# Kernel optimization log

Hardware: AMD Instinct MI355X
Metric: run time of the kernel (lower is better)

The kernel has to match this reference:

```python
import jax, jax.numpy as jnp
import numpy as np

D_MODEL = 2048
N_HEADS = 16
HEAD_DIM = D_MODEL // N_HEADS
B, T = 2, 2048


def setup_inputs() -> dict:
    key = jax.random.key(0)
    ks = jax.random.split(key, 7)
    s = 0.02
    return {
        "x": jax.random.normal(ks[0], (B, T, D_MODEL), dtype=jnp.float32),
        "w_qkv": jax.random.normal(ks[1], (D_MODEL, 3 * D_MODEL), dtype=jnp.float32) * s,
        "w_proj": jax.random.normal(ks[2], (D_MODEL, D_MODEL), dtype=jnp.float32) * s,
        "w_ff1": jax.random.normal(ks[3], (D_MODEL, 4 * D_MODEL), dtype=jnp.float32) * s,
        "b_ff1": jnp.zeros((4 * D_MODEL,), dtype=jnp.float32),
        "w_ff2": jax.random.normal(ks[4], (4 * D_MODEL, D_MODEL), dtype=jnp.float32) * s,
        "b_ff2": jnp.zeros((D_MODEL,), dtype=jnp.float32),
    }


def reference(x, w_qkv, w_proj, w_ff1, b_ff1, w_ff2, b_ff2):
    Bs, Ts, C = x.shape
    H, hd = N_HEADS, HEAD_DIM
    # fused qkv projection
    qkv = jnp.einsum("btc,cd->btd", x, w_qkv)
    q, k, v = jnp.split(qkv, 3, axis=-1)
    # (B, T, C) -> (B, H, T, hd)
    q = q.reshape(Bs, Ts, H, hd).transpose(0, 2, 1, 3)
    k = k.reshape(Bs, Ts, H, hd).transpose(0, 2, 1, 3)
    v = v.reshape(Bs, Ts, H, hd).transpose(0, 2, 1, 3)
    # paged KV write + gather round-trip (empty cache, n_kv_head == n_heads)
    # is the identity on k, v; attention is causal SDPA over the full cache.
    scale = 1.0 / jnp.sqrt(jnp.asarray(hd, dtype=x.dtype))
    scores = jnp.einsum("bhqd,bhkd->bhqk", q, k) * scale
    causal = jnp.tril(jnp.ones((Ts, Ts), dtype=bool))
    scores = jnp.where(causal, scores, jnp.finfo(scores.dtype).min)
    attn = jax.nn.softmax(scores, axis=-1)
    out = jnp.einsum("bhqk,bhkd->bhqd", attn, v)  # (B, H, T, hd)
    out = out.transpose(0, 2, 1, 3).reshape(Bs, Ts, C)
    attn_out = jnp.einsum("btc,cd->btd", out, w_proj)
    # feed-forward with exact GELU (torch nn.GELU default)
    h = jax.nn.gelu(jnp.einsum("btc,cf->btf", x, w_ff1) + b_ff1, approximate=False)
    ff_out = jnp.einsum("btf,fc->btc", h, w_ff2) + b_ff2
    return x + attn_out + ff_out
```

## Files before the change

### kernel.cpp

```cpp
#include <hip/hip_runtime.h>
#include <hip/hip_bf16.h>
#include <cmath>

typedef __bf16 bf16x8 __attribute__((ext_vector_type(8)));
typedef float f32x4 __attribute__((ext_vector_type(4)));
typedef unsigned short u16;
typedef unsigned int u32;

#define DEV __device__ __forceinline__

static constexpr int BB = 2;
static constexpr int T = 2048;
static constexpr int DM = 2048;
static constexpr int NH = 16;
static constexpr int HD = 128;
static constexpr int FF = 8192;
static constexpr int M = BB * T;
static constexpr int NQKV = 3 * DM;

DEV u16 f2b(float f) {
  u32 u = __builtin_bit_cast(u32, f);
  u = (u + 0x7FFFu + ((u >> 16) & 1u)) >> 16;
  return (u16)u;
}
DEV float b2f(u16 h) {
  u32 u = ((u32)h) << 16;
  return __builtin_bit_cast(float, u);
}

DEV void gload16(const u16* g, const u16* l) {
  __builtin_amdgcn_global_load_lds(
      (const __attribute__((address_space(1))) void*)(uintptr_t)g,
      (__attribute__((address_space(3))) void*)(unsigned)(uintptr_t)l,
      16, 0, 0);
}


__global__ void cvt_f32_to_bf16(const float* __restrict__ in, u16* __restrict__ out, int n4) {
  int i = blockIdx.x * blockDim.x + threadIdx.x;
  if (i >= n4) return;
  float4 v = reinterpret_cast<const float4*>(in)[i];
  ushort4 o;
  o.x = f2b(v.x); o.y = f2b(v.y); o.z = f2b(v.z); o.w = f2b(v.w);
  reinterpret_cast<ushort4*>(out)[i] = o;
}

__global__ void transpose_cvt(const float* __restrict__ W, u16* __restrict__ Wt, int K, int N) {
  __shared__ float tile[32][33];
  int nb = blockIdx.x * 32, kb = blockIdx.y * 32;
  int r = threadIdx.x >> 3;
  int c4 = (threadIdx.x & 7) * 4;
  float4 v = *reinterpret_cast<const float4*>(&W[(size_t)(kb + r) * N + nb + c4]);
  tile[r][c4] = v.x; tile[r][c4 + 1] = v.y; tile[r][c4 + 2] = v.z; tile[r][c4 + 3] = v.w;
  __syncthreads();
  ushort4 o;
  o.x = f2b(tile[c4][r]);     o.y = f2b(tile[c4 + 1][r]);
  o.z = f2b(tile[c4 + 2][r]); o.w = f2b(tile[c4 + 3][r]);
  *reinterpret_cast<ushort4*>(&Wt[(size_t)(nb + r) * K + kb + c4]) = o;
}

__global__ void ff2_reduce(const float* __restrict__ p0, const float* __restrict__ p1,
                           const float* __restrict__ bias, const float* __restrict__ x,
                           const u16* __restrict__ ap, float* __restrict__ out) {
  int i = blockIdx.x * blockDim.x + threadIdx.x;
  float4 a = reinterpret_cast<const float4*>(p0)[i];
  float4 b = reinterpret_cast<const float4*>(p1)[i];
  float4 xx = reinterpret_cast<const float4*>(x)[i];
  float4 bi = reinterpret_cast<const float4*>(bias)[i & (DM / 4 - 1)];
  ushort4 a4 = reinterpret_cast<const ushort4*>(ap)[i];
  float4 o;
  o.x = a.x + b.x + bi.x + xx.x + b2f(a4.x);
  o.y = a.y + b.y + bi.y + xx.y + b2f(a4.y);
  o.z = a.z + b.z + bi.z + xx.z + b2f(a4.z);
  o.w = a.w + b.w + bi.w + xx.w + b2f(a4.w);
  reinterpret_cast<float4*>(out)[i] = o;
}

template <int EPI>
__global__ __launch_bounds__(512, 2) void gemm8(
    const u16* __restrict__ A, const u16* __restrict__ Bt, int Ndim,
    int Kstride, int Klen, int gx, int tpp,
    u16* __restrict__ out_bf, float* __restrict__ p0, float* __restrict__ p1,
    const float* __restrict__ bias) {
  __shared__ __align__(16) u16 lds[2 * 32768];
  const int t = threadIdx.x;
  const int nwg = gridDim.x, cpx = nwg >> 3;
  const int wg = (blockIdx.x & 7) * cpx + (blockIdx.x >> 3);
  const int part = wg / tpp, tid = wg % tpp;
  const int m0 = (tid / gx) * 256, n0 = (tid % gx) * 256;
  const int wave = t >> 6, lane = t & 63;
  const int wm = wave >> 2, wn = wave & 3;
  const int lr = lane & 15, lk = lane >> 4;

  const int srow = t >> 3;
  const int sc8 = ((t & 7) ^ (srow & 7)) * 8;
  const u16* gA = &A[(size_t)(m0 + srow) * Kstride + (size_t)part * Klen + sc8];
  const u16* gB = &Bt[(size_t)(n0 + srow) * Kstride + (size_t)part * Klen + sc8];
  const int wls = wave * 512;

  u16* buf0 = lds;
  u16* buf1 = lds + 32768;

#define STAGE_A(buf, h, kt)                                                      \
  {                                                                              \
    gload16(gA + (size_t)((h) * 128) * Kstride + (kt) * 64,                      \
            (buf) + (h) * 8192 + wls);                                           \
    gload16(gA + (size_t)((h) * 128 + 64) * Kstride + (kt) * 64,                 \
            (buf) + (h) * 8192 + 4096 + wls);                                    \
  }
#define STAGE_B(buf, h, kt)                                                      \
  {                                                                              \
    gload16(gB + (size_t)((h) * 128) * Kstride + (kt) * 64,                      \
            (buf) + 16384 + (h) * 8192 + wls);                                   \
    gload16(gB + (size_t)((h) * 128 + 64) * Kstride + (kt) * 64,                 \
            (buf) + 16384 + (h) * 8192 + 4096 + wls);                            \
  }
#define PH_PRE                          \
  __builtin_amdgcn_sched_barrier(0);    \
  __builtin_amdgcn_s_barrier();         \
  __builtin_amdgcn_sched_barrier(0);    \
  __builtin_amdgcn_s_setprio(1);
#define PH_POST                         \
  __builtin_amdgcn_s_setprio(0);        \
  __builtin_amdgcn_sched_barrier(0);    \
  __builtin_amdgcn_s_barrier();         \
  __builtin_amdgcn_sched_barrier(0);

  const int NT = Klen >> 6;

  STAGE_A(buf0, 0, 0); STAGE_A(buf0, 1, 0);
  STAGE_B(buf0, 0, 0); STAGE_B(buf0, 1, 0);
  STAGE_A(buf1, 0, 1); STAGE_B(buf1, 0, 1);
  __builtin_amdgcn_sched_barrier(0);
  asm volatile("s_waitcnt vmcnt(4)" ::: "memory");
  __builtin_amdgcn_s_barrier();
  __builtin_amdgcn_sched_barrier(0);

  f32x4 acc[8][4] = {};
  const int aBase = (wm * 128 + lr) * 64;
  const int bBase = 16384 + (wn * 64 + lr) * 64;
  const int c0 = (lk ^ (lr & 7)) * 8;
  const int c1 = ((4 + lk) ^ (lr & 7)) * 8;

  u16* cur = buf0;
  u16* alt = buf1;
  bf16x8 af[4][2], bq0[2][2], bq1[2][2];

  for (int kt = 0; kt < NT; ++kt) {
#pragma unroll
    for (int i = 0; i < 4; ++i) {
      af[i][0] = *(const bf16x8*)&cur[aBase + i * 1024 + c0];
      af[i][1] = *(const bf16x8*)&cur[aBase + i * 1024 + c1];
    }
#pragma unroll
    for (int j = 0; j < 2; ++j) {
      bq0[j][0] = *(const bf16x8*)&cur[bBase + j * 1024 + c0];
      bq0[j][1] = *(const bf16x8*)&cur[bBase + j * 1024 + c1];
    }
    if (kt + 1 < NT) STAGE_A(alt, 1, kt + 1);
    PH_PRE;
#pragma unroll
    for (int i = 0; i < 4; ++i)
#pragma unroll
      for (int j = 0; j < 2; ++j)
#pragma unroll
        for (int kk = 0; kk < 2; ++kk)
          acc[i][j] = __builtin_amdgcn_mfma_f32_16x16x32_bf16(af[i][kk], bq0[j][kk], acc[i][j], 0, 0, 0);
    PH_POST;
#pragma unroll
    for (int j = 0; j < 2; ++j) {
      bq1[j][0] = *(const bf16x8*)&cur[bBase + (2 + j) * 1024 + c0];
      bq1[j][1] = *(const bf16x8*)&cur[bBase + (2 + j) * 1024 + c1];
    }
    if (kt + 1 < NT) STAGE_B(alt, 1, kt + 1);
    PH_PRE;
#pragma unroll
    for (int i = 0; i < 4; ++i)
#pragma unroll
      for (int j = 0; j < 2; ++j)
#pragma unroll
        for (int kk = 0; kk < 2; ++kk)
          acc[i][2 + j] = __builtin_amdgcn_mfma_f32_16x16x32_bf16(af[i][kk], bq1[j][kk], acc[i][2 + j], 0, 0, 0);
    PH_POST;
#pragma unroll
    for (int i = 0; i < 4; ++i) {
      af[i][0] = *(const bf16x8*)&cur[aBase + (4 + i) * 1024 + c0];
      af[i][1] = *(const bf16x8*)&cur[aBase + (4 + i) * 1024 + c1];
    }
    if (kt + 2 < NT) STAGE_A(cur, 0, kt + 2);
    PH_PRE;
#pragma unroll
    for (int i = 0; i < 4; ++i)
#pragma unroll
      for (int j = 0; j < 2; ++j)
#pragma unroll
        for (int kk = 0; kk < 2; ++kk)
          acc[4 + i][2 + j] = __builtin_amdgcn_mfma_f32_16x16x32_bf16(af[i][kk], bq1[j][kk], acc[4 + i][2 + j], 0, 0, 0);
    PH_POST;
    if (kt + 2 < NT) STAGE_B(cur, 0, kt + 2);
    PH_PRE;
#pragma unroll
    for (int i = 0; i < 4; ++i)
#pragma unroll
      for (int j = 0; j < 2; ++j)
#pragma unroll
        for (int kk = 0; kk < 2; ++kk)
          acc[4 + i][j] = __builtin_amdgcn_mfma_f32_16x16x32_bf16(af[i][kk], bq0[j][kk], acc[4 + i][j], 0, 0, 0);
    __builtin_amdgcn_s_setprio(0);
    __builtin_amdgcn_sched_barrier(0);
    if (kt + 2 < NT)      asm volatile("s_waitcnt vmcnt(4)" ::: "memory");
    else if (kt + 1 < NT) asm volatile("s_waitcnt vmcnt(0)" ::: "memory");
    __builtin_amdgcn_s_barrier();
    __builtin_amdgcn_sched_barrier(0);
    u16* tmp = cur; cur = alt; alt = tmp;
  }
#undef STAGE_A
#undef STAGE_B
#undef PH_PRE
#undef PH_POST

  float* pout = (part == 0) ? p0 : p1;
#pragma unroll
  for (int i = 0; i < 8; ++i) {
#pragma unroll
    for (int j = 0; j < 4; ++j) {
#pragma unroll
      for (int r = 0; r < 4; ++r) {
        int gr = m0 + wm * 128 + i * 16 + (lane >> 4) * 4 + r;
        int gc = n0 + wn * 64 + j * 16 + (lane & 15);
        float v = acc[i][j][r];
        if constexpr (EPI == 0) {
          int part_ = gc >> 11, cc = gc & 2047;
          int head = cc >> 7, d = cc & 127;
          int b = gr >> 11, tt = gr & 2047;
          out_bf[(size_t)part_ * M * DM + (((size_t)(b * NH + head) * T + tt) * HD + d)] = f2b(v);
        } else if constexpr (EPI == 2) {
          v += bias[gc];
          float u = v * (v * v * 0.044715f + 1.0f) * 0.7978845608028654f;
          float e = exp2f(u * 2.885390081777927f);
          float th = 1.0f - 2.0f / (e + 1.0f);
          v = 0.5f * v * (1.0f + th);
          out_bf[(size_t)gr * Ndim + gc] = f2b(v);
        } else {
          pout[(size_t)gr * Ndim + gc] = v;
        }
      }
    }
  }
}

template <int EPI>
__global__ __launch_bounds__(512, 4) void gemm_bf16(
    const u16* __restrict__ A, const u16* __restrict__ Bt, int Ndim, int K, int gx,
    u16* __restrict__ out_bf, float* __restrict__ out_f32,
    const float* __restrict__ bias,
    const float* __restrict__ resid_f32, const u16* __restrict__ resid_bf) {
  __shared__ __align__(16) u16 lds[3 * (256 + 128) * 32];
  const int t = threadIdx.x;
  const int nwg = gridDim.x, cpx = nwg >> 3;
  const int wg = (blockIdx.x & 7) * cpx + (blockIdx.x >> 3);
  const int m0 = (wg / gx) * 256, n0 = (wg % gx) * 128;
  const int wave = t >> 6, lane = t & 63;
  const int wm = wave >> 1, wn = wave & 1;
  const int lr = lane & 15, lk = lane >> 4;

  u16* cA = lds;                   u16* cB = lds + 8192;
  u16* nA = lds + 12288;           u16* nB = lds + 12288 + 8192;
  u16* sA = lds + 2 * 12288;       u16* sB = lds + 2 * 12288 + 8192;

  const int sk = ((lane & 3) ^ ((lane >> 3) & 3)) * 8;
  const u16* gA0 = &A[(size_t)(m0 + wave * 16 + (lane >> 2)) * K + sk];
  const u16* gA1 = gA0 + (size_t)128 * K;
  const u16* gB0 = &Bt[(size_t)(n0 + wave * 16 + (lane >> 2)) * K + sk];

  const int wbase = wave * 512;

  auto stage = [&](u16* dA, u16* dB) {
    gload16(gA0, dA + wbase);
    gload16(gA1, dA + 4096 + wbase);
    gload16(gB0, dB + wbase);
    gA0 += 32; gA1 += 32; gB0 += 32;
  };

  const int NT = K >> 5;

  stage(cA, cB);
  stage(nA, nB);
  __builtin_amdgcn_sched_barrier(0);
  asm volatile("s_waitcnt vmcnt(3)" ::: "memory");
  __builtin_amdgcn_s_barrier();
  __builtin_amdgcn_sched_barrier(0);

  f32x4 acc[4][4] = {};
  const int rcol = (lk ^ ((lr >> 1) & 3)) * 8;

  for (int kt = 0; kt < NT; ++kt) {
    if (kt + 2 < NT) stage(sA, sB);
    bf16x8 af[4], bfr[4];
#pragma unroll
    for (int i = 0; i < 4; ++i) {
      af[i]  = *reinterpret_cast<const bf16x8*>(&cA[(wm * 64 + i * 16 + lr) * 32 + rcol]);
      bfr[i] = *reinterpret_cast<const bf16x8*>(&cB[(wn * 64 + i * 16 + lr) * 32 + rcol]);
    }
#pragma unroll
    for (int i = 0; i < 4; ++i)
#pragma unroll
      for (int j = 0; j < 4; ++j)
        acc[i][j] = __builtin_amdgcn_mfma_f32_16x16x32_bf16(af[i], bfr[j], acc[i][j], 0, 0, 0);
    if (kt + 1 < NT) {
      __builtin_amdgcn_sched_barrier(0);
      if (kt + 2 < NT) asm volatile("s_waitcnt vmcnt(3)" ::: "memory");
      else             asm volatile("s_waitcnt vmcnt(0)" ::: "memory");
      __builtin_amdgcn_s_barrier();
      __builtin_amdgcn_sched_barrier(0);
      u16* tA = cA; u16* tB = cB;
      cA = nA; cB = nB; nA = sA; nB = sB; sA = tA; sB = tB;
    }
  }

#pragma unroll
  for (int i = 0; i < 4; ++i) {
#pragma unroll
    for (int j = 0; j < 4; ++j) {
#pragma unroll
      for (int r = 0; r < 4; ++r) {
        int gr = m0 + wm * 64 + i * 16 + (lane >> 4) * 4 + r;
        int gc = n0 + wn * 64 + j * 16 + (lane & 15);
        float v = acc[i][j][r];
        if constexpr (EPI == 1) {
          out_bf[(size_t)gr * Ndim + gc] = f2b(v);
        } else if constexpr (EPI == 3) {
          v += bias[gc] + resid_f32[(size_t)gr * Ndim + gc] + b2f(resid_bf[(size_t)gr * Ndim + gc]);
          out_f32[(size_t)gr * Ndim + gc] = v;
        } else {
          int hh = gr >> 7, d = gr & 127;
          int b = gc >> 11, tt = gc & 2047;
          out_bf[((size_t)(b * NH + hh) * HD + d) * T + tt] = f2b(v);
        }
      }
    }
  }
}

__global__ __launch_bounds__(256) void attn_fwd(
    const u16* __restrict__ qg, const u16* __restrict__ kg,
    const u16* __restrict__ vt, u16* __restrict__ outg) {
  __shared__ __align__(16) u16 lK[2][64 * 128];
  __shared__ __align__(16) u16 lVt[2][128 * 64];
  __shared__ __align__(16) u16 lP[4][16 * 72];
  const int t = threadIdx.x;
  const int qi = gridDim.x - 1 - blockIdx.x;
  const int bh = blockIdx.y;
  const int wv = t >> 6, lane = t & 63;
  const int lc = lane & 15, lg = lane >> 4;
  const size_t base = (size_t)bh * T * HD;
  const size_t vbase = (size_t)bh * HD * T;
  const int q0 = qi * 64;

  bf16x8 qf[4];
#pragma unroll
  for (int kk = 0; kk < 4; ++kk)
    qf[kk] = *reinterpret_cast<const bf16x8*>(
        &qg[base + (size_t)(q0 + wv * 16 + lc) * HD + kk * 32 + lg * 8]);

  f32x4 oacc[8] = {};
  float mrow[4], lrow[4];
#pragma unroll
  for (int r = 0; r < 4; ++r) { mrow[r] = -INFINITY; lrow[r] = 0.f; }

  auto stageKV = [&](int kt, int b) {
#pragma unroll
    for (int h = 0; h < 4; ++h) {
      int c = t + h * 256;
      int row = c >> 4;
      int sb = ((c & 15) * 16) ^ ((row & 7) << 4);
      gload16(&kg[base + (size_t)(kt * 64 + row) * HD + (sb >> 1)],
              (const u16*)((const char*)lK[b] + (h * 256 + wv * 64) * 16));
    }
#pragma unroll
    for (int h = 0; h < 4; ++h) {
      int c = t + h * 256;
      int row = c >> 3;
      int sb = ((c & 7) * 16) ^ ((row & 7) << 4);
      gload16(&vt[vbase + (size_t)row * T + kt * 64 + (sb >> 1)],
              (const u16*)((const char*)lVt[b] + (h * 256 + wv * 64) * 16));
    }
  };

  const float scaleL = 0.08838834764831845f * 1.4426950408889634f;
  const int ntiles = qi + 1;

  stageKV(0, 0);
  __builtin_amdgcn_sched_barrier(0);
  asm volatile("s_waitcnt vmcnt(0)" ::: "memory");
  __builtin_amdgcn_s_barrier();
  __builtin_amdgcn_sched_barrier(0);

  for (int kt = 0; kt < ntiles; ++kt) {
    const int cb = kt & 1;
    if (kt + 1 < ntiles) stageKV(kt + 1, cb ^ 1);
    const u16* lKc = lK[cb];
    const u16* lVc = lVt[cb];

    f32x4 s[4] = {};
    __builtin_amdgcn_s_setprio(1);
#pragma unroll
    for (int nf = 0; nf < 4; ++nf) {
      int krow = nf * 16 + lc;
#pragma unroll
      for (int kk = 0; kk < 4; ++kk) {
        int dbyte = kk * 64 + lg * 16;
        bf16x8 kf = *reinterpret_cast<const bf16x8*>(
            reinterpret_cast<const char*>(lKc) + krow * 256 + (dbyte ^ ((krow & 7) << 4)));
        s[nf] = __builtin_amdgcn_mfma_f32_16x16x32_bf16(qf[kk], kf, s[nf], 0, 0, 0);
      }
    }
    __builtin_amdgcn_s_setprio(0);

    float rmax[4];
#pragma unroll
    for (int r = 0; r < 4; ++r) rmax[r] = -INFINITY;
#pragma unroll
    for (int nf = 0; nf < 4; ++nf) {
      int col = kt * 64 + nf * 16 + lc;
#pragma unroll
      for (int r = 0; r < 4; ++r) {
        int row = q0 + wv * 16 + lg * 4 + r;
        float sv = s[nf][r] * scaleL;
        if (col > row) sv = -INFINITY;
        s[nf][r] = sv;
        rmax[r] = fmaxf(rmax[r], sv);
      }
    }
#pragma unroll
    for (int mk = 1; mk < 16; mk <<= 1)
#pragma unroll
      for (int r = 0; r < 4; ++r)
        rmax[r] = fmaxf(rmax[r], __shfl_xor(rmax[r], mk));

    int need = 0;
#pragma unroll
    for (int r = 0; r < 4; ++r) need |= (rmax[r] > mrow[r] + 11.5f) ? 1 : 0;
    if (__any(need)) {
      float corr[4];
#pragma unroll
      for (int r = 0; r < 4; ++r) {
        float mnew = fmaxf(mrow[r], rmax[r]);
        corr[r] = exp2f(mrow[r] - mnew);
        mrow[r] = mnew;
        lrow[r] *= corr[r];
      }
#pragma unroll
      for (int dc = 0; dc < 8; ++dc)
#pragma unroll
        for (int r = 0; r < 4; ++r) oacc[dc][r] *= corr[r];
    }

#pragma unroll
    for (int nf = 0; nf < 4; ++nf) {
#pragma unroll
      for (int r = 0; r < 4; ++r) {
        float p = exp2f(s[nf][r] - mrow[r]);
        lrow[r] += p;
        lP[wv][(lg * 4 + r) * 72 + nf * 16 + lc] = f2b(p);
      }
    }
    bf16x8 pa[2];
#pragma unroll
    for (int kk = 0; kk < 2; ++kk)
      pa[kk] = *reinterpret_cast<const bf16x8*>(&lP[wv][lc * 72 + kk * 32 + lg * 8]);
    __builtin_amdgcn_s_setprio(1);
#pragma unroll
    for (int dc = 0; dc < 8; ++dc) {
#pragma unroll
      for (int kk = 0; kk < 2; ++kk) {
        int vrow = dc * 16 + lc;
        int off = (kk * 64 + lg * 16) ^ ((vrow & 7) << 4);
        bf16x8 vf = *reinterpret_cast<const bf16x8*>(
            reinterpret_cast<const char*>(lVc) + vrow * 128 + off);
        oacc[dc] = __builtin_amdgcn_mfma_f32_16x16x32_bf16(pa[kk], vf, oacc[dc], 0, 0, 0);
      }
    }
    __builtin_amdgcn_s_setprio(0);

    __builtin_amdgcn_sched_barrier(0);
    if (kt + 1 < ntiles) asm volatile("s_waitcnt vmcnt(0)" ::: "memory");
    __builtin_amdgcn_s_barrier();
    __builtin_amdgcn_sched_barrier(0);
  }

#pragma unroll
  for (int mk = 1; mk < 16; mk <<= 1)
#pragma unroll
    for (int r = 0; r < 4; ++r) lrow[r] += __shfl_xor(lrow[r], mk);

  const int b = bh >> 4, hh = bh & 15;
#pragma unroll
  for (int dc = 0; dc < 8; ++dc)
#pragma unroll
    for (int r = 0; r < 4; ++r) {
      int tt = q0 + wv * 16 + lg * 4 + r;
      int d = dc * 16 + lc;
      float o = oacc[dc][r] / lrow[r];
      outg[(size_t)(b * T + tt) * DM + hh * HD + d] = f2b(o);
    }
}


extern "C" void kernel_launch(void* const* d_in, const int* in_sizes, int n_in,
                              void* d_out, int out_size, void* d_ws, size_t ws_size,
                              hipStream_t stream) {
  const float* x      = (const float*)d_in[0];
  const float* w_qkv  = (const float*)d_in[1];
  const float* w_proj = (const float*)d_in[2];
  const float* w_ff1  = (const float*)d_in[3];
  const float* b_ff1  = (const float*)d_in[4];
  const float* w_ff2  = (const float*)d_in[5];
  const float* b_ff2  = (const float*)d_in[6];
  float* out = (float*)d_out;

  u16* ws = (u16*)d_ws;
  size_t o = 0;
  u16* x_bf      = ws + o; o += (size_t)M * DM;
  u16* wqkv_t    = ws + o; o += (size_t)NQKV * DM;
  u16* wproj_t   = ws + o; o += (size_t)DM * DM;
  u16* wff1_t    = ws + o; o += (size_t)FF * DM;
  u16* wff2_t    = ws + o; o += (size_t)DM * FF;
  u16* attn_proj = ws + o; o += (size_t)M * DM;
  u16* qbuf      = ws + o;
  u16* kbuf      = qbuf + (size_t)M * DM;
  u16* vtbuf     = kbuf + (size_t)M * DM;
  u16* attn_out  = vtbuf + (size_t)M * DM;
  u16* hbuf      = qbuf;

  float* p0 = (float*)ws;
  float* p1 = (float*)wff1_t;

  cvt_f32_to_bf16<<<(M * DM / 4 + 255) / 256, 256, 0, stream>>>(x, x_bf, M * DM / 4);
  transpose_cvt<<<dim3(NQKV / 32, DM / 32), 256, 0, stream>>>(w_qkv, wqkv_t, DM, NQKV);
  transpose_cvt<<<dim3(DM / 32, DM / 32), 256, 0, stream>>>(w_proj, wproj_t, DM, DM);
  transpose_cvt<<<dim3(FF / 32, DM / 32), 256, 0, stream>>>(w_ff1, wff1_t, DM, FF);
  transpose_cvt<<<dim3(DM / 32, FF / 32), 256, 0, stream>>>(w_ff2, wff2_t, FF, DM);

  gemm8<0><<<256, 512, 0, stream>>>(x_bf, wqkv_t, 4096, DM, DM, 16, 256,
                                    qbuf, nullptr, nullptr, nullptr);

  gemm_bf16<4><<<256, 512, 0, stream>>>(
      wqkv_t + (size_t)4096 * DM, x_bf, M, DM, 32, vtbuf, nullptr, nullptr, nullptr, nullptr);

  attn_fwd<<<dim3(T / 64, BB * NH), 256, 0, stream>>>(qbuf, kbuf, vtbuf, attn_out);

  gemm_bf16<1><<<256, 512, 0, stream>>>(
      attn_out, wproj_t, DM, DM, 16, attn_proj, nullptr, nullptr, nullptr, nullptr);

  gemm8<2><<<512, 512, 0, stream>>>(x_bf, wff1_t, FF, DM, DM, 32, 512,
                                    hbuf, nullptr, nullptr, b_ff1);

  gemm8<5><<<256, 512, 0, stream>>>(hbuf, wff2_t, DM, FF, 4096, 8, 128,
                                    nullptr, p0, p1, nullptr);

  ff2_reduce<<<M * DM / 4 / 256, 256, 0, stream>>>(p0, p1, b_ff2, x, attn_proj, out);
}
```

Before: 646.4 us.

## Store Q/K/V in MFMA fragment layout and run LDS-free attention

The QKV and V-transpose GEMM epilogues now write Q, K and V directly in a pre-tiled 32x32 MFMA fragment order. This lets a new attention kernel load operands straight from global memory into registers with no LDS staging or barriers. Each wave works independently on 32 query rows, using 32x32x16 MFMAs and register shuffles to rebuild the P operand. The cost is that K/V tiles are no longer shared across waves through LDS, so global and L2 traffic goes up. The causal work split also changes to 32-row blocks per wave, with the grid launched as T/128 blocks.

```diff
diff --git a/kernel.cpp b/kernel.cpp
--- a/kernel.cpp
+++ b/kernel.cpp
@@ -4,6 +4,7 @@
 
 typedef __bf16 bf16x8 __attribute__((ext_vector_type(8)));
 typedef float f32x4 __attribute__((ext_vector_type(4)));
+typedef float f32x16 __attribute__((ext_vector_type(16)));
 typedef unsigned short u16;
 typedef unsigned int u32;
 
@@ -233,7 +234,10 @@
           int part_ = gc >> 11, cc = gc & 2047;
           int head = cc >> 7, d = cc & 127;
           int b = gr >> 11, tt = gr & 2047;
-          out_bf[(size_t)part_ * M * DM + (((size_t)(b * NH + head) * T + tt) * HD + d)] = f2b(v);
+          int bh = b * NH + head;
+          size_t addr = (((size_t)(bh * 64 + (tt >> 5)) * 8 + (d >> 4)) * 512)
+                        + ((tt & 31) + ((d >> 3) & 1) * 32) * 8 + (d & 7);
+          out_bf[(size_t)part_ * M * DM + addr] = f2b(v);
         } else if constexpr (EPI == 2) {
           v += bias[gc];
           float u = v * (v * v * 0.044715f + 1.0f) * 0.7978845608028654f;
@@ -335,175 +339,130 @@
         } else {
           int hh = gr >> 7, d = gr & 127;
           int b = gc >> 11, tt = gc & 2047;
-          out_bf[((size_t)(b * NH + hh) * HD + d) * T + tt] = f2b(v);
+          int bh = b * NH + hh;
+          size_t addr = (((size_t)(bh * 128 + (tt >> 4)) * 4 + (d >> 5)) * 512)
+                        + ((d & 31) + ((tt >> 3) & 1) * 32) * 8 + (tt & 7);
+          out_bf[addr] = f2b(v);
         }
       }
     }
   }
 }
 
-__global__ __launch_bounds__(256) void attn_fwd(
-    const u16* __restrict__ qg, const u16* __restrict__ kg,
-    const u16* __restrict__ vt, u16* __restrict__ outg) {
-  __shared__ __align__(16) u16 lK[2][64 * 128];
-  __shared__ __align__(16) u16 lVt[2][128 * 64];
-  __shared__ __align__(16) u16 lP[4][16 * 72];
-  const int t = threadIdx.x;
+__global__ __launch_bounds__(256) void attn_frag(
+    const u16* __restrict__ qf_, const u16* __restrict__ kf_,
+    const u16* __restrict__ vf_, u16* __restrict__ outg) {
+  const int l = threadIdx.x & 63;
+  const int wq = threadIdx.x >> 6;
+  const int bh = blockIdx.y;
   const int qi = gridDim.x - 1 - blockIdx.x;
-  const int bh = blockIdx.y;
-  const int wv = t >> 6, lane = t & 63;
-  const int lc = lane & 15, lg = lane >> 4;
-  const size_t base = (size_t)bh * T * HD;
-  const size_t vbase = (size_t)bh * HD * T;
-  const int q0 = qi * 64;
-
-  bf16x8 qf[4];
-#pragma unroll
-  for (int kk = 0; kk < 4; ++kk)
-    qf[kk] = *reinterpret_cast<const bf16x8*>(
-        &qg[base + (size_t)(q0 + wv * 16 + lc) * HD + kk * 32 + lg * 8]);
-
-  f32x4 oacc[8] = {};
-  float mrow[4], lrow[4];
-#pragma unroll
-  for (int r = 0; r < 4; ++r) { mrow[r] = -INFINITY; lrow[r] = 0.f; }
-
-  auto stageKV = [&](int kt, int b) {
-#pragma unroll
-    for (int h = 0; h < 4; ++h) {
-      int c = t + h * 256;
-      int row = c >> 4;
-      int sb = ((c & 15) * 16) ^ ((row & 7) << 4);
-      gload16(&kg[base + (size_t)(kt * 64 + row) * HD + (sb >> 1)],
-              (const u16*)((const char*)lK[b] + (h * 256 + wv * 64) * 16));
-    }
-#pragma unroll
-    for (int h = 0; h < 4; ++h) {
-      int c = t + h * 256;
-      int row = c >> 3;
-      int sb = ((c & 7) * 16) ^ ((row & 7) << 4);
-      gload16(&vt[vbase + (size_t)row * T + kt * 64 + (sb >> 1)],
-              (const u16*)((const char*)lVt[b] + (h * 256 + wv * 64) * 16));
-    }
-  };
-
+  const int qb = qi * 4 + wq;
+  const int h = l >> 5, ln = l & 31;
+  const int qrow = qb * 32 + ln;
+
+  const u16* qbase = qf_ + ((size_t)(bh * 64 + qb) * 8) * 512 + l * 8;
+  bf16x8 qf[8];
+#pragma unroll
+  for (int s = 0; s < 8; ++s)
+    qf[s] = *reinterpret_cast<const bf16x8*>(qbase + s * 512);
+
+  f32x16 acc0 = {}, acc1 = {}, acc2 = {}, acc3 = {};
+  float mrow = -INFINITY, lrow = 0.f;
   const float scaleL = 0.08838834764831845f * 1.4426950408889634f;
-  const int ntiles = qi + 1;
-
-  stageKV(0, 0);
-  __builtin_amdgcn_sched_barrier(0);
-  asm volatile("s_waitcnt vmcnt(0)" ::: "memory");
-  __builtin_amdgcn_s_barrier();
-  __builtin_amdgcn_sched_barrier(0);
+  const int ntiles = qb + 1;
 
   for (int kt = 0; kt < ntiles; ++kt) {
-    const int cb = kt & 1;
-    if (kt + 1 < ntiles) stageKV(kt + 1, cb ^ 1);
-    const u16* lKc = lK[cb];
-    const u16* lVc = lVt[cb];
-
-    f32x4 s[4] = {};
-    __builtin_amdgcn_s_setprio(1);
-#pragma unroll
-    for (int nf = 0; nf < 4; ++nf) {
-      int krow = nf * 16 + lc;
-#pragma unroll
-      for (int kk = 0; kk < 4; ++kk) {
-        int dbyte = kk * 64 + lg * 16;
-        bf16x8 kf = *reinterpret_cast<const bf16x8*>(
-            reinterpret_cast<const char*>(lKc) + krow * 256 + (dbyte ^ ((krow & 7) << 4)));
-        s[nf] = __builtin_amdgcn_mfma_f32_16x16x32_bf16(qf[kk], kf, s[nf], 0, 0, 0);
+    const u16* kbase = kf_ + ((size_t)(bh * 64 + kt) * 8) * 512 + l * 8;
+    f32x16 sa = {};
+#pragma unroll
+    for (int s = 0; s < 8; ++s) {
+      bf16x8 kf = *reinterpret_cast<const bf16x8*>(kbase + s * 512);
+      sa = __builtin_amdgcn_mfma_f32_32x32x16_bf16(kf, qf[s], sa, 0, 0, 0);
+    }
+
+    float p[16];
+    float lmax = -INFINITY;
+    const bool diag = (kt == qb);
+#pragma unroll
+    for (int r = 0; r < 16; ++r) {
+      float sv = sa[r] * scaleL;
+      if (diag) {
+        int kv = kt * 32 + (r & 3) + 8 * (r >> 2) + 4 * h;
+        if (kv > qrow) sv = -INFINITY;
       }
-    }
-    __builtin_amdgcn_s_setprio(0);
-
-    float rmax[4];
-#pragma unroll
-    for (int r = 0; r < 4; ++r) rmax[r] = -INFINITY;
-#pragma unroll
-    for (int nf = 0; nf < 4; ++nf) {
-      int col = kt * 64 + nf * 16 + lc;
-#pragma unroll
-      for (int r = 0; r < 4; ++r) {
-        int row = q0 + wv * 16 + lg * 4 + r;
-        float sv = s[nf][r] * scaleL;
-        if (col > row) sv = -INFINITY;
-        s[nf][r] = sv;
-        rmax[r] = fmaxf(rmax[r], sv);
+      p[r] = sv;
+      lmax = fmaxf(lmax, sv);
+    }
+    float rmax = fmaxf(lmax, __shfl_xor(lmax, 32));
+
+    if (__any(rmax > mrow + 11.5f)) {
+      float mnew = fmaxf(mrow, rmax);
+      float corr = exp2f(mrow - mnew);
+      mrow = mnew;
+      lrow *= corr;
+#pragma unroll
+      for (int r = 0; r < 16; ++r) {
+        float cr = __shfl(corr, (r & 3) + 8 * (r >> 2) + 4 * h);
+        acc0[r] *= cr; acc1[r] *= cr; acc2[r] *= cr; acc3[r] *= cr;
       }
     }
-#pragma unroll
-    for (int mk = 1; mk < 16; mk <<= 1)
-#pragma unroll
-      for (int r = 0; r < 4; ++r)
-        rmax[r] = fmaxf(rmax[r], __shfl_xor(rmax[r], mk));
-
-    int need = 0;
-#pragma unroll
-    for (int r = 0; r < 4; ++r) need |= (rmax[r] > mrow[r] + 11.5f) ? 1 : 0;
-    if (__any(need)) {
-      float corr[4];
-#pragma unroll
-      for (int r = 0; r < 4; ++r) {
-        float mnew = fmaxf(mrow[r], rmax[r]);
-        corr[r] = exp2f(mrow[r] - mnew);
-        mrow[r] = mnew;
-        lrow[r] *= corr[r];
-      }
-#pragma unroll
-      for (int dc = 0; dc < 8; ++dc)
-#pragma unroll
-        for (int r = 0; r < 4; ++r) oacc[dc][r] *= corr[r];
-    }
-
-#pragma unroll
-    for (int nf = 0; nf < 4; ++nf) {
-#pragma unroll
-      for (int r = 0; r < 4; ++r) {
-        float p = exp2f(s[nf][r] - mrow[r]);
-        lrow[r] += p;
-        lP[wv][(lg * 4 + r) * 72 + nf * 16 + lc] = f2b(p);
-      }
-    }
-    bf16x8 pa[2];
-#pragma unroll
-    for (int kk = 0; kk < 2; ++kk)
-      pa[kk] = *reinterpret_cast<const bf16x8*>(&lP[wv][lc * 72 + kk * 32 + lg * 8]);
-    __builtin_amdgcn_s_setprio(1);
-#pragma unroll
-    for (int dc = 0; dc < 8; ++dc) {
-#pragma unroll
-      for (int kk = 0; kk < 2; ++kk) {
-        int vrow = dc * 16 + lc;
-        int off = (kk * 64 + lg * 16) ^ ((vrow & 7) << 4);
-        bf16x8 vf = *reinterpret_cast<const bf16x8*>(
-            reinterpret_cast<const char*>(lVc) + vrow * 128 + off);
-        oacc[dc] = __builtin_amdgcn_mfma_f32_16x16x32_bf16(pa[kk], vf, oacc[dc], 0, 0, 0);
-      }
-    }
-    __builtin_amdgcn_s_setprio(0);
-
-    __builtin_amdgcn_sched_barrier(0);
-    if (kt + 1 < ntiles) asm volatile("s_waitcnt vmcnt(0)" ::: "memory");
-    __builtin_amdgcn_s_barrier();
-    __builtin_amdgcn_sched_barrier(0);
-  }
-
-#pragma unroll
-  for (int mk = 1; mk < 16; mk <<= 1)
-#pragma unroll
-    for (int r = 0; r < 4; ++r) lrow[r] += __shfl_xor(lrow[r], mk);
+
+    float ls = 0.f;
+#pragma unroll
+    for (int r = 0; r < 16; ++r) {
+      p[r] = exp2f(p[r] - mrow);
+      ls += p[r];
+    }
+    lrow += ls + __shfl_xor(ls, 32);
+
+    u32 w[8];
+#pragma unroll
+    for (int c = 0; c < 8; ++c)
+      asm("v_cvt_pk_bf16_f32 %0, %1, %2" : "=v"(w[c]) : "v"(p[2 * c]), "v"(p[2 * c + 1]));
+    u32 x[8];
+#pragma unroll
+    for (int c = 0; c < 8; ++c) x[c] = (u32)__shfl_xor((int)w[c], 32);
+    uint4 A0, A1;
+    A0.x = h ? x[2] : w[0]; A0.y = h ? x[3] : w[1];
+    A0.z = h ? w[2] : x[0]; A0.w = h ? w[3] : x[1];
+    A1.x = h ? x[6] : w[4]; A1.y = h ? x[7] : w[5];
+    A1.z = h ? w[6] : x[4]; A1.w = h ? w[7] : x[5];
+    bf16x8 pa0 = __builtin_bit_cast(bf16x8, A0);
+    bf16x8 pa1 = __builtin_bit_cast(bf16x8, A1);
+
+    const u16* vbase = vf_ + ((size_t)(bh * 128 + kt * 2) * 4) * 512 + l * 8;
+    bf16x8 v0, v1;
+    v0 = *reinterpret_cast<const bf16x8*>(vbase + 0 * 512);
+    v1 = *reinterpret_cast<const bf16x8*>(vbase + 4 * 512);
+    acc0 = __builtin_amdgcn_mfma_f32_32x32x16_bf16(pa0, v0, acc0, 0, 0, 0);
+    acc0 = __builtin_amdgcn_mfma_f32_32x32x16_bf16(pa1, v1, acc0, 0, 0, 0);
+    v0 = *reinterpret_cast<const bf16x8*>(vbase + 1 * 512);
+    v1 = *reinterpret_cast<const bf16x8*>(vbase + 5 * 512);
+    acc1 = __builtin_amdgcn_mfma_f32_32x32x16_bf16(pa0, v0, acc1, 0, 0, 0);
+    acc1 = __builtin_amdgcn_mfma_f32_32x32x16_bf16(pa1, v1, acc1, 0, 0, 0);
+    v0 = *reinterpret_cast<const bf16x8*>(vbase + 2 * 512);
+    v1 = *reinterpret_cast<const bf16x8*>(vbase + 6 * 512);
+    acc2 = __builtin_amdgcn_mfma_f32_32x32x16_bf16(pa0, v0, acc2, 0, 0, 0);
+    acc2 = __builtin_amdgcn_mfma_f32_32x32x16_bf16(pa1, v1, acc2, 0, 0, 0);
+    v0 = *reinterpret_cast<const bf16x8*>(vbase + 3 * 512);
+    v1 = *reinterpret_cast<const bf16x8*>(vbase + 7 * 512);
+    acc3 = __builtin_amdgcn_mfma_f32_32x32x16_bf16(pa0, v0, acc3, 0, 0, 0);
+    acc3 = __builtin_amdgcn_mfma_f32_32x32x16_bf16(pa1, v1, acc3, 0, 0, 0);
+  }
 
   const int b = bh >> 4, hh = bh & 15;
 #pragma unroll
-  for (int dc = 0; dc < 8; ++dc)
-#pragma unroll
-    for (int r = 0; r < 4; ++r) {
-      int tt = q0 + wv * 16 + lg * 4 + r;
-      int d = dc * 16 + lc;
-      float o = oacc[dc][r] / lrow[r];
-      outg[(size_t)(b * T + tt) * DM + hh * HD + d] = f2b(o);
-    }
+  for (int r = 0; r < 16; ++r) {
+    int qr = (r & 3) + 8 * (r >> 2) + 4 * h;
+    float lr = __shfl(lrow, qr);
+    float rl = 1.0f / lr;
+    int tt = qb * 32 + qr;
+    size_t rowoff = ((size_t)(b * T + tt)) * DM + hh * HD + ln;
+    outg[rowoff + 0]  = f2b(acc0[r] * rl);
+    outg[rowoff + 32] = f2b(acc1[r] * rl);
+    outg[rowoff + 64] = f2b(acc2[r] * rl);
+    outg[rowoff + 96] = f2b(acc3[r] * rl);
+  }
 }
 
 
@@ -548,7 +507,7 @@
   gemm_bf16<4><<<256, 512, 0, stream>>>(
       wqkv_t + (size_t)4096 * DM, x_bf, M, DM, 32, vtbuf, nullptr, nullptr, nullptr, nullptr);
 
-  attn_fwd<<<dim3(T / 64, BB * NH), 256, 0, stream>>>(qbuf, kbuf, vtbuf, attn_out);
+  attn_frag<<<dim3(T / 128, BB * NH), 256, 0, stream>>>(qbuf, kbuf, vtbuf, attn_out);
 
   gemm_bf16<1><<<256, 512, 0, stream>>>(
       attn_out, wproj_t, DM, DM, 16, attn_proj, nullptr, nullptr, nullptr, nullptr);
```

New measurement: 636.8 us. No clear change (-1.5%).
